# Optimization experiments

Hardware: AMD Instinct MI355X
Metric: run time of the kernel (lower is better)

The kernel has to match this reference:

```python
import jax, jax.numpy as jnp
import numpy as np
from jax import lax

K = 11  # kernel_size
THRESH = 0.2  # focus_threshold default
DN = ('NCHW', 'OIHW', 'NCHW')


def conv3(x, w, b):
    # 3x3 conv, stride 1, SAME padding (padding=1 in torch)
    return lax.conv_general_dilated(x, w, (1, 1), 'SAME', dimension_numbers=DN) + b[None, :, None, None]


def apply_separable_filters(rgb, kh, kv, k):
    # rgb [B,3,H,W]; kh, kv [B,k,H,W] softmaxed per-pixel 1D kernels
    pad = k // 2
    B, C, H, W = rgb.shape
    # horizontal pass: gather k horizontally-shifted views, weight by kh
    xp = jnp.pad(rgb, ((0, 0), (0, 0), (0, 0), (pad, pad)))
    ph = jnp.stack([xp[:, :, :, i:i + W] for i in range(k)], axis=2)  # [B,3,k,H,W]
    h = jnp.einsum('bckhw,bkhw->bchw', ph, kh)
    # vertical pass
    hp = jnp.pad(h, ((0, 0), (0, 0), (pad, pad), (0, 0)))
    pv = jnp.stack([hp[:, :, i:i + H, :] for i in range(k)], axis=2)  # [B,3,k,H,W]
    return jnp.einsum('bckhw,bkhw->bchw', pv, kv)


def get_depth_mask(depth, threshold):
    # binary in-focus mask: pixels closer than threshold stay sharp
    return (depth > threshold).astype(depth.dtype)


def setup_inputs() -> dict:
    key = jax.random.key(0)
    ks = jax.random.split(key, 18)
    B, H, W = 8, 256, 256
    s = 0.05
    f32 = jnp.float32
    inp = {
        'rgb': jax.random.uniform(ks[0], (B, 3, H, W), f32),
        'depth': jax.random.uniform(ks[1], (B, 1, H, W), f32),
        'w1': jax.random.normal(ks[2], (64, 4, 3, 3), f32) * s, 'b1': jnp.zeros(64, f32),
        'w2': jax.random.normal(ks[3], (64, 64, 3, 3), f32) * s, 'b2': jnp.zeros(64, f32),
        'w3': jax.random.normal(ks[4], (128, 64, 3, 3), f32) * s, 'b3': jnp.zeros(128, f32),
        'w4': jax.random.normal(ks[5], (128, 128, 3, 3), f32) * s, 'b4': jnp.zeros(128, f32),
        'w5': jax.random.normal(ks[6], (64, 128, 3, 3), f32) * s, 'b5': jnp.zeros(64, f32),
        'wh': jax.random.normal(ks[7], (K, 64, 3, 3), f32) * s, 'bh': jnp.zeros(K, f32),
        'wv': jax.random.normal(ks[8], (K, 64, 3, 3), f32) * s, 'bv': jnp.zeros(K, f32),
    }
    return inp


def reference(rgb, depth, w1, b1, w2, b2, w3, b3, w4, b4, w5, b5, wh, bh, wv, bv):
    x = jnp.concatenate([rgb, depth], axis=1)  # [B,4,H,W]
    f = jax.nn.relu(conv3(x, w1, b1))
    f = jax.nn.relu(conv3(f, w2, b2))
    f = jax.nn.relu(conv3(f, w3, b3))
    f = jax.nn.relu(conv3(f, w4, b4))
    f = jax.nn.relu(conv3(f, w5, b5))
    kh = jax.nn.softmax(conv3(f, wh, bh), axis=1)
    kv = jax.nn.softmax(conv3(f, wv, bv), axis=1)
    blurred = apply_separable_filters(rgb, kh, kv, K)
    mask = get_depth_mask(depth, THRESH)
    final = mask * rgb + (1.0 - mask) * blurred
    return (final, blurred, kh, kv, mask)
```

## Files before the change

kernel.cpp:

```cpp
#include <hip/hip_runtime.h>
#include <hip/hip_bf16.h>
#include <math.h>

#define HH 256
#define WW 256
#define HW (HH*WW)
#define BB 8

typedef __hip_bfloat16 bf16;
typedef __attribute__((ext_vector_type(8))) short short8;
typedef __attribute__((ext_vector_type(4))) float f32x4;
typedef __attribute__((ext_vector_type(16))) float f32x16;

#define AS1 __attribute__((address_space(1)))
#define AS3 __attribute__((address_space(3)))


template<int CO, int CI>
__global__ __launch_bounds__(256) void reorder_w_cl(const float* __restrict__ w,
                                                    bf16* __restrict__ wr)
{
    int idx = blockIdx.x * 256 + threadIdx.x;
    if (idx >= 9 * CO * CI) return;
    int j    = idx & 7;
    int lane = (idx >> 3) & 63;
    int nt   = (idx >> 9) % (CO / 32);
    int rest = idx / (512 * (CO / 32));
    int ks   = rest & 1;
    int tt   = (rest >> 1) % 9;
    int kc   = rest / 18;
    int co = nt * 32 + (lane & 31);
    int ci = kc * 32 + ks * 16 + (lane >> 5) * 8 + j;
    wr[idx] = __float2bfloat16(w[((size_t)co * CI + ci) * 9 + tt]);
}

__global__ __launch_bounds__(256) void reorder_w_head2_lm(const float* __restrict__ wh,
                                                          const float* __restrict__ wv,
                                                          bf16* __restrict__ wr)
{
    int idx = blockIdx.x * 256 + threadIdx.x;
    if (idx >= 2 * 9 * 2 * 64 * 8) return;
    int j    = idx & 7;
    int lane = (idx >> 3) & 63;
    int fr   = (idx >> 9) & 1;
    int t    = (idx >> 10) % 9;
    int kc   = (idx >> 10) / 9;
    int co   = fr * 16 + (lane & 15);
    int ci   = kc * 32 + (lane >> 4) * 8 + j;
    const float* src = (co < 16) ? wh : wv;
    int c = co & 15;
    float v = (c < 11) ? src[((size_t)c * 64 + ci) * 9 + t] : 0.0f;
    wr[idx] = __float2bfloat16(v);
}

template<int ROWS, int TPB>
__device__ __forceinline__ void zero_oob(bf16* __restrict__ s0,
                                         bf16* __restrict__ s1,
                                         int tid, int x0, int y0)
{
    constexpr int UNITS = (ROWS + 2) * 264;
    const short8 z8 = {0,0,0,0,0,0,0,0};
    for (int e = tid; e < UNITS; e += TPB) {
        int row = e / 264, rem = e - row * 264;
        int px = rem >> 2;
        int yy = y0 - 1 + row, xx = x0 - 1 + px;
        if (yy < 0 || yy >= HH || xx < 0 || xx >= WW) {
            *(short8*)(s0 + (size_t)e * 8) = z8;
            *(short8*)(s1 + (size_t)e * 8) = z8;
        }
    }
}

template<int CIN, int ROWS, int TPB>
__device__ __forceinline__ void stage_async(const bf16* __restrict__ in_i,
                                            bf16* __restrict__ slab,
                                            int tid, int x0, int y0, int k0)
{
    constexpr int UNITS = (ROWS + 2) * 264;
    const int lane = tid & 63;
    const int wb   = tid - lane;
    for (int base = wb; base < UNITS; base += TPB) {
        int e = base + lane;
        int row = e / 264, rem = e - row * 264;
        int px = rem >> 2, slot = rem & 3;
        int seg = slot ^ ((px >> 1) & 3);
        int yy = y0 - 1 + row, xx = x0 - 1 + px;
        bool ok = (e < UNITS) && (yy >= 0) && (yy < HH) && (xx >= 0) && (xx < WW);
        if (ok) {
            const bf16* g = in_i + ((size_t)(yy * WW + xx)) * CIN + k0 + seg * 8;
            __builtin_amdgcn_global_load_lds((const AS1 void*)g,
                                             (AS3 void*)(slab + (size_t)base * 8),
                                             16, 0, 0);
        }
    }
}

template<int COC>
__global__ __launch_bounds__(256) void conv3x3_first(const float* __restrict__ rgb,
                                                     const float* __restrict__ depth,
                                                     const float* __restrict__ w,
                                                     const float* __restrict__ bias,
                                                     bf16* __restrict__ out, int b0)
{
    const int tid = threadIdx.x;
    const int img = blockIdx.y >> 6;
    const int b   = b0 + img;
    const int x = blockIdx.x * 64 + (tid & 63);
    const int y = (blockIdx.y & 63) * 4 + (tid >> 6);

    const bool vy0 = (y > 0), vy2 = (y < HH - 1);
    const bool vx0 = (x > 0), vx2 = (x < WW - 1);
    bool val[9];
    int  off[9];
    {
        int t = 0;
        for (int dy = -1; dy <= 1; ++dy)
            for (int dx = -1; dx <= 1; ++dx) {
                val[t] = (dy < 0 ? vy0 : (dy > 0 ? vy2 : true)) &&
                         (dx < 0 ? vx0 : (dx > 0 ? vx2 : true));
                off[t] = dy * WW + dx;
                ++t;
            }
    }

    float acc[COC];
#pragma unroll
    for (int j = 0; j < COC; ++j) acc[j] = bias[j];

    const int p0 = y * WW + x;
#pragma unroll
    for (int ci = 0; ci < 4; ++ci) {
        const float* p = (ci < 3) ? (rgb + ((size_t)(b * 3 + ci)) * HW + p0)
                                  : (depth + (size_t)b * HW + p0);
        float v[9];
#pragma unroll
        for (int t = 0; t < 9; ++t)
            v[t] = val[t] ? p[off[t]] : 0.0f;

        const float* wp = w + (size_t)ci * 9;
#pragma unroll
        for (int j = 0; j < COC; ++j) {
            const float* wj = wp + (size_t)j * 4 * 9;
#pragma unroll
            for (int t = 0; t < 9; ++t)
                acc[j] = fmaf(wj[t], v[t], acc[j]);
        }
    }

    bf16* op = out + (size_t)img * HW * 64 + (size_t)p0 * 64;
#pragma unroll
    for (int g = 0; g < COC / 8; ++g) {
        short8 s;
#pragma unroll
        for (int j = 0; j < 8; ++j) {
            bf16 h = __float2bfloat16(fmaxf(acc[g * 8 + j], 0.0f));
            s[j] = *reinterpret_cast<short*>(&h);
        }
        *(short8*)(op + g * 8) = s;
    }
}

template<int CIN, int COUT, int WPB>
__global__ __launch_bounds__(256, WPB) void conv_mfma_v12(const bf16* __restrict__ in,
                                                          const bf16* __restrict__ wrb,
                                                          const float* __restrict__ bias,
                                                          bf16* __restrict__ out)
{
    constexpr int NCH  = CIN / 32;
    constexpr int NTT  = COUT / 64;
    constexpr int NTOT = COUT / 32;
    constexpr int SLAB = 6 * 66 * 32;
    __shared__ bf16 slab[2 * SLAB];

    const int tid  = threadIdx.x;
    const int lane = tid & 63;
    const int wv   = tid >> 6;
    const int ng   = wv & 1;
    const int rg   = wv >> 1;
    const int ln31 = lane & 31;
    const int oct  = lane >> 5;
    const int img  = blockIdx.y >> 6;
    const int x0   = blockIdx.x * 64;
    const int y0   = (blockIdx.y & 63) * 4;

    const bf16* in_i  = in  + (size_t)img * HW * CIN;
    bf16*       out_i = out + (size_t)img * HW * COUT;

    f32x16 acc[4][NTT];
#pragma unroll
    for (int mt = 0; mt < 4; ++mt)
#pragma unroll
        for (int nt = 0; nt < NTT; ++nt)
#pragma unroll
            for (int j = 0; j < 16; ++j) acc[mt][nt][j] = 0.0f;

    zero_oob<4, 256>(slab, slab + SLAB, tid, x0, y0);
    stage_async<CIN, 4, 256>(in_i, slab, tid, x0, y0, 0);

    int cur = 0;
    for (int kc = 0; kc < NCH; ++kc) {
        __syncthreads();
        if (kc + 1 < NCH)
            stage_async<CIN, 4, 256>(in_i, slab + (size_t)(cur ^ 1) * SLAB,
                                     tid, x0, y0, (kc + 1) * 32);

        const bf16* sb = slab + (size_t)cur * SLAB;
#pragma unroll
        for (int t = 0; t < 9; ++t) {
            const int dy = t / 3 - 1, dx = t % 3 - 1;
#pragma unroll
            for (int ks = 0; ks < 2; ++ks) {
                short8 a[4];
#pragma unroll
                for (int mt = 0; mt < 4; ++mt) {
                    const int srow = 2 * rg + (mt >> 1) + dy + 1;
                    const int px   = (mt & 1) * 32 + ln31 + dx + 1;
                    const int slot = (ks * 2 + oct) ^ ((px >> 1) & 3);
                    a[mt] = *(const short8*)(sb + (srow * 66 + px) * 32 + slot * 8);
                }
#pragma unroll
                for (int nt = 0; nt < NTT; ++nt) {
                    const int gnt = ng * NTT + nt;
                    short8 bfr = *(const short8*)(wrb
                        + ((size_t)((((kc * 9 + t) * 2 + ks) * NTOT + gnt) * 64 + lane)) * 8);
#pragma unroll
                    for (int mt = 0; mt < 4; ++mt)
                        acc[mt][nt] = __builtin_amdgcn_mfma_f32_32x32x16_bf16(
                                          a[mt], bfr, acc[mt][nt], 0, 0, 0);
                }
            }
        }
        cur ^= 1;
    }

#pragma unroll
    for (int nt = 0; nt < NTT; ++nt) {
        const int co = (ng * NTT + nt) * 32 + ln31;
        const float bb = bias[co];
#pragma unroll
        for (int mt = 0; mt < 4; ++mt) {
            const int r  = 2 * rg + (mt >> 1);
            const int xb = x0 + (mt & 1) * 32;
#pragma unroll
            for (int j = 0; j < 16; ++j) {
                const int m = (j & 3) + 8 * (j >> 2) + 4 * oct;
                const float v = fmaxf(acc[mt][nt][j] + bb, 0.0f);
                out_i[((size_t)(y0 + r) * WW + (xb + m)) * COUT + co] = __float2bfloat16(v);
            }
        }
    }
}

template<int CIN, int COUT, int WPB>
__global__ __launch_bounds__(256, WPB) void conv_mfma_v13(const bf16* __restrict__ in,
                                                          const bf16* __restrict__ wrb,
                                                          const float* __restrict__ bias,
                                                          bf16* __restrict__ out)
{
    constexpr int NCH  = CIN / 32;
    constexpr int NTT  = COUT / 64;
    constexpr int NTOT = COUT / 32;
    constexpr int SLAB = 6 * 66 * 32;
    __shared__ bf16 slab[2 * SLAB];

    const int tid  = threadIdx.x;
    const int lane = tid & 63;
    const int wv   = tid >> 6;
    const int ng   = wv & 1;
    const int rg   = wv >> 1;
    const int ln31 = lane & 31;
    const int oct  = lane >> 5;
    const int img  = blockIdx.y >> 6;
    const int x0   = blockIdx.x * 64;
    const int y0   = (blockIdx.y & 63) * 4;

    const bf16* in_i  = in  + (size_t)img * HW * CIN;
    bf16*       out_i = out + (size_t)img * HW * COUT;

    f32x16 acc[4][NTT];
#pragma unroll
    for (int mt = 0; mt < 4; ++mt)
#pragma unroll
        for (int nt = 0; nt < NTT; ++nt)
#pragma unroll
            for (int j = 0; j < 16; ++j) acc[mt][nt][j] = 0.0f;

    zero_oob<4, 256>(slab, slab + SLAB, tid, x0, y0);
    stage_async<CIN, 4, 256>(in_i, slab, tid, x0, y0, 0);

    int cur = 0;
    for (int kc = 0; kc < NCH; ++kc) {
        __syncthreads();
        if (kc + 1 < NCH)
            stage_async<CIN, 4, 256>(in_i, slab + (size_t)(cur ^ 1) * SLAB,
                                     tid, x0, y0, (kc + 1) * 32);

        const bf16* sb = slab + (size_t)cur * SLAB;
#pragma unroll
        for (int dxi = 0; dxi < 3; ++dxi) {
            const int dx = dxi - 1;
#pragma unroll
            for (int ks = 0; ks < 2; ++ks) {
                short8 af[4][2];
#pragma unroll
                for (int s = 0; s < 4; ++s)
#pragma unroll
                    for (int mx = 0; mx < 2; ++mx) {
                        const int px   = mx * 32 + ln31 + dx + 1;
                        const int slot = (ks * 2 + oct) ^ ((px >> 1) & 3);
                        af[s][mx] = *(const short8*)(sb + ((2 * rg + s) * 66 + px) * 32 + slot * 8);
                    }
#pragma unroll
                for (int dyi = 0; dyi < 3; ++dyi) {
                    const int t = dyi * 3 + dxi;
#pragma unroll
                    for (int nt = 0; nt < NTT; ++nt) {
                        const int gnt = ng * NTT + nt;
                        short8 bfr = *(const short8*)(wrb
                            + ((size_t)((((kc * 9 + t) * 2 + ks) * NTOT + gnt) * 64 + lane)) * 8);
#pragma unroll
                        for (int mt = 0; mt < 4; ++mt)
                            acc[mt][nt] = __builtin_amdgcn_mfma_f32_32x32x16_bf16(
                                              af[(mt >> 1) + dyi][mt & 1], bfr, acc[mt][nt], 0, 0, 0);
                    }
                }
            }
        }
        cur ^= 1;
    }

#pragma unroll
    for (int nt = 0; nt < NTT; ++nt) {
        const int co = (ng * NTT + nt) * 32 + ln31;
        const float bb = bias[co];
#pragma unroll
        for (int mt = 0; mt < 4; ++mt) {
            const int r  = 2 * rg + (mt >> 1);
            const int xb = x0 + (mt & 1) * 32;
#pragma unroll
            for (int j = 0; j < 16; ++j) {
                const int m = (j & 3) + 8 * (j >> 2) + 4 * oct;
                const float v = fmaxf(acc[mt][nt][j] + bb, 0.0f);
                out_i[((size_t)(y0 + r) * WW + (xb + m)) * COUT + co] = __float2bfloat16(v);
            }
        }
    }
}

__global__ __launch_bounds__(256, 2) void head_mfma2(const bf16* __restrict__ in,
                                                     const bf16* __restrict__ wrp,
                                                     const float* __restrict__ bh,
                                                     const float* __restrict__ bv,
                                                     float* __restrict__ kh_base,
                                                     float* __restrict__ kv_base,
                                                     int b0)
{
    constexpr int SLABH = 6 * 66 * 32;
    __shared__ bf16  slab[2 * SLABH];
    __shared__ float smx[4][64][17];

    const int tid  = threadIdx.x;
    const int lane = tid & 63;
    const int wv   = tid >> 6;
    const int m    = lane & 15;
    const int q    = lane >> 4;
    const int img  = blockIdx.y >> 6;
    const int x0   = blockIdx.x * 64;
    const int y0   = (blockIdx.y & 63) * 4;
    const int y    = y0 + wv;

    const bf16* in_i = in + (size_t)img * HW * 64;

    f32x4 acc[4][2];
#pragma unroll
    for (int f = 0; f < 4; ++f) { acc[f][0] = (f32x4){0.f,0.f,0.f,0.f}; acc[f][1] = (f32x4){0.f,0.f,0.f,0.f}; }

    zero_oob<4, 256>(slab, slab + SLABH, tid, x0, y0);
    stage_async<64, 4, 256>(in_i, slab, tid, x0, y0, 0);

    int cur = 0;
    for (int kc = 0; kc < 2; ++kc) {
        __syncthreads();
        if (kc == 0)
            stage_async<64, 4, 256>(in_i, slab + SLABH, tid, x0, y0, 32);

        const bf16* sb = slab + (size_t)cur * SLABH;
#pragma unroll
        for (int t = 0; t < 9; ++t) {
            const int dy = t / 3 - 1, dx = t % 3 - 1;
            const int srow = wv + dy + 1;
            short8 b0f = *(const short8*)(wrp + ((size_t)(((kc * 9 + t) * 2 + 0) * 64 + lane)) * 8);
            short8 b1f = *(const short8*)(wrp + ((size_t)(((kc * 9 + t) * 2 + 1) * 64 + lane)) * 8);
#pragma unroll
            for (int f = 0; f < 4; ++f) {
                const int px = f * 16 + m + dx + 1;
                const int slot = q ^ ((px >> 1) & 3);
                short8 a = *(const short8*)(sb + (srow * 66 + px) * 32 + slot * 8);
                acc[f][0] = __builtin_amdgcn_mfma_f32_16x16x32_bf16(a, b0f, acc[f][0], 0, 0, 0);
                acc[f][1] = __builtin_amdgcn_mfma_f32_16x16x32_bf16(a, b1f, acc[f][1], 0, 0, 0);
            }
        }
        cur ^= 1;
    }

#pragma unroll
    for (int head = 0; head < 2; ++head) {
        const float* bias = head ? bv : bh;
        const float bb = (m < 11) ? bias[m] : 0.0f;
#pragma unroll
        for (int f = 0; f < 4; ++f)
#pragma unroll
            for (int r = 0; r < 4; ++r)
                smx[wv][f * 16 + q * 4 + r][m] = acc[f][head][r] + bb;

        float v[11];
#pragma unroll
        for (int j = 0; j < 11; ++j) v[j] = smx[wv][lane][j];
        float mx = v[0];
#pragma unroll
        for (int j = 1; j < 11; ++j) mx = fmaxf(mx, v[j]);
        float s = 0.0f;
#pragma unroll
        for (int j = 0; j < 11; ++j) { v[j] = expf(v[j] - mx); s += v[j]; }
        const float inv = 1.0f / s;

        float* op = (head ? kv_base : kh_base) + (size_t)(b0 + img) * 11 * HW
                    + (size_t)y * WW + x0 + lane;
#pragma unroll
        for (int j = 0; j < 11; ++j)
            op[(size_t)j * HW] = v[j] * inv;
    }
}

__global__ __launch_bounds__(256) void hpass(const float* __restrict__ rgb,
                                             const float* __restrict__ kh,
                                             float* __restrict__ h)
{
    int idx = blockIdx.x * 256 + threadIdx.x;
    int b = idx >> 16;
    int p = idx & (HW - 1);
    int y = p >> 8;
    int x = p & 255;

    float kw[11];
#pragma unroll
    for (int i = 0; i < 11; ++i) kw[i] = kh[((size_t)(b * 11 + i)) * HW + p];

#pragma unroll
    for (int c = 0; c < 3; ++c) {
        const float* rp = rgb + ((size_t)(b * 3 + c)) * HW + (size_t)y * WW;
        float s = 0.0f;
#pragma unroll
        for (int i = 0; i < 11; ++i) {
            int xx = x + i - 5;
            if (xx >= 0 && xx < WW) s = fmaf(kw[i], rp[xx], s);
        }
        h[((size_t)(b * 3 + c)) * HW + p] = s;
    }
}

__global__ __launch_bounds__(256) void vpass_compose(const float* __restrict__ h,
                                                     const float* __restrict__ kv,
                                                     const float* __restrict__ rgb,
                                                     const float* __restrict__ depth,
                                                     float* __restrict__ fin,
                                                     float* __restrict__ blur,
                                                     float* __restrict__ masko)
{
    int idx = blockIdx.x * 256 + threadIdx.x;
    int b = idx >> 16;
    int p = idx & (HW - 1);
    int y = p >> 8;
    int x = p & 255;

    float kw[11];
#pragma unroll
    for (int i = 0; i < 11; ++i) kw[i] = kv[((size_t)(b * 11 + i)) * HW + p];

    float d = depth[idx];
    float mk = (d > 0.2f) ? 1.0f : 0.0f;
    masko[idx] = mk;

#pragma unroll
    for (int c = 0; c < 3; ++c) {
        const float* hp = h + ((size_t)(b * 3 + c)) * HW + x;
        float s = 0.0f;
#pragma unroll
        for (int i = 0; i < 11; ++i) {
            int yy = y + i - 5;
            if (yy >= 0 && yy < HH) s = fmaf(kw[i], hp[(size_t)yy * WW], s);
        }
        size_t o = ((size_t)(b * 3 + c)) * HW + p;
        blur[o] = s;
        fin[o] = mk * rgb[o] + (1.0f - mk) * s;
    }
}

extern "C" void kernel_launch(void* const* d_in, const int* in_sizes, int n_in,
                              void* d_out, int out_size, void* d_ws, size_t ws_size,
                              hipStream_t stream)
{
    const float* rgb   = (const float*)d_in[0];
    const float* depth = (const float*)d_in[1];
    const float* w1 = (const float*)d_in[2];  const float* b1 = (const float*)d_in[3];
    const float* w2 = (const float*)d_in[4];  const float* b2 = (const float*)d_in[5];
    const float* w3 = (const float*)d_in[6];  const float* b3 = (const float*)d_in[7];
    const float* w4 = (const float*)d_in[8];  const float* b4 = (const float*)d_in[9];
    const float* w5 = (const float*)d_in[10]; const float* b5 = (const float*)d_in[11];
    const float* wh = (const float*)d_in[12]; const float* bh = (const float*)d_in[13];
    const float* wv = (const float*)d_in[14]; const float* bv = (const float*)d_in[15];

    float* out    = (float*)d_out;
    float* fin_o  = out;
    float* blur_o = out + 1572864;
    float* kh_o   = out + 3145728;
    float* kv_o   = out + 8912896;
    float* mask_o = out + 14680064;

    const size_t perG = (size_t)HW * 2 * (128 + 64 + 128);
    const size_t wsz  = (size_t)1 * 1024 * 1024;
    int G = 1;
    if (ws_size >= 8 * perG + wsz) G = 8;
    else if (ws_size >= 4 * perG + wsz) G = 4;
    else if (ws_size >= 2 * perG + wsz) G = 2;

    char* ws = (char*)d_ws;
    const size_t szA = (size_t)G * HW * 128 * 2;
    const size_t szB = (size_t)G * HW * 64 * 2;
    const size_t szC = (size_t)G * HW * 128 * 2;
    bf16* bufA = (bf16*)ws;
    bf16* bufB = (bf16*)(ws + szA);
    bf16* bufC = (bf16*)(ws + szA + szB);
    float* hbuf = (float*)bufC;

    bf16* w2r  = (bf16*)(ws + szA + szB + szC);
    bf16* w3r  = w2r + 9 * 64 * 64;
    bf16* w4r  = w3r + 9 * 128 * 64;
    bf16* w5r  = w4r + 9 * 128 * 128;
    bf16* whvr = w5r + 9 * 64 * 128;

    dim3 blk(256);

    reorder_w_cl<64, 64>  <<<dim3((9*64*64   + 255) / 256), blk, 0, stream>>>(w2, w2r);
    reorder_w_cl<128, 64> <<<dim3((9*128*64  + 255) / 256), blk, 0, stream>>>(w3, w3r);
    reorder_w_cl<128, 128><<<dim3((9*128*128 + 255) / 256), blk, 0, stream>>>(w4, w4r);
    reorder_w_cl<64, 128> <<<dim3((9*64*128  + 255) / 256), blk, 0, stream>>>(w5, w5r);
    reorder_w_head2_lm    <<<dim3((18432     + 255) / 256), blk, 0, stream>>>(wh, wv, whvr);

    for (int b0 = 0; b0 < BB; b0 += G) {
        conv3x3_first<64><<<dim3(4, 64 * G, 1), blk, 0, stream>>>(rgb, depth, w1, b1, bufA, b0);
        conv_mfma_v13<64, 64, 3>  <<<dim3(4, 64 * G), blk, 0, stream>>>(bufA, w2r, b2, bufB);
        conv_mfma_v12<64, 128, 2> <<<dim3(4, 64 * G), blk, 0, stream>>>(bufB, w3r, b3, bufC);
        conv_mfma_v12<128, 128, 2><<<dim3(4, 64 * G), blk, 0, stream>>>(bufC, w4r, b4, bufA);
        conv_mfma_v13<128, 64, 3> <<<dim3(4, 64 * G), blk, 0, stream>>>(bufA, w5r, b5, bufB);
        head_mfma2<<<dim3(4, 64 * G), blk, 0, stream>>>(bufB, whvr, bh, bv, kh_o, kv_o, b0);
    }

    hpass<<<dim3(2048), blk, 0, stream>>>(rgb, kh_o, hbuf);
    vpass_compose<<<dim3(2048), blk, 0, stream>>>(hbuf, kv_o, rgb, depth,
                                                  fin_o, blur_o, mask_o);
}
```

Measured before the change: 777.5 us.

## Move first conv to MFMA via padded 8-channel bf16 input and reordered weights

Replaces the scalar FMA first 3x3 conv (4 input channels to 64) with a pre-pass that writes a zero-padded 258x258 bf16 image holding 8 channels per pixel (RGB, depth, zeros). An MFMA kernel then packs two taps per 16-wide K step and runs 5 K steps of 32x32x16 bf16 MFMA. This removes the per-thread 36x64 FMA loop and the boundary checks. In exchange it adds an extra kernel launch and a padded buffer write and read, reuses the bufC workspace as the padded buffer, and writes output with scattered 2-byte stores.

```diff
diff --git a/kernel.cpp b/kernel.cpp
--- a/kernel.cpp
+++ b/kernel.cpp
@@ -6,6 +6,8 @@
 #define WW 256
 #define HW (HH*WW)
 #define BB 8
+#define PW 258
+#define PHW2 (PW*PW)
 
 typedef __hip_bfloat16 bf16;
 typedef __attribute__((ext_vector_type(8))) short short8;
@@ -51,6 +53,113 @@
     int c = co & 15;
     float v = (c < 11) ? src[((size_t)c * 64 + ci) * 9 + t] : 0.0f;
     wr[idx] = __float2bfloat16(v);
+}
+
+__global__ __launch_bounds__(256) void reorder_w1_mfma(const float* __restrict__ w,
+                                                       bf16* __restrict__ wr)
+{
+    int idx = blockIdx.x * 256 + threadIdx.x;
+    if (idx >= 5 * 2 * 64 * 8) return;
+    int j    = idx & 7;
+    int lane = (idx >> 3) & 63;
+    int nt   = (idx >> 9) & 1;
+    int km   = idx >> 10;
+    int co   = nt * 32 + (lane & 31);
+    int tap  = km * 2 + (lane >> 5);
+    float v  = (tap < 9 && j < 4) ? w[((size_t)co * 4 + j) * 9 + tap] : 0.0f;
+    wr[idx] = __float2bfloat16(v);
+}
+
+__global__ __launch_bounds__(256) void pad8_rgbd(const float* __restrict__ rgb,
+                                                 const float* __restrict__ depth,
+                                                 bf16* __restrict__ p8,
+                                                 int b0, int G)
+{
+    int idx = blockIdx.x * 256 + threadIdx.x;
+    if (idx >= G * PHW2) return;
+    int img = idx / PHW2;
+    int rem = idx - img * PHW2;
+    int r = rem / PW, c = rem - r * PW;
+    int y = r - 1, x = c - 1;
+    short8 s = {0,0,0,0,0,0,0,0};
+    if (y >= 0 && y < HH && x >= 0 && x < WW) {
+        const int b = b0 + img;
+        const int p0 = y * WW + x;
+        float v[4];
+        v[0] = rgb[((size_t)(b * 3 + 0)) * HW + p0];
+        v[1] = rgb[((size_t)(b * 3 + 1)) * HW + p0];
+        v[2] = rgb[((size_t)(b * 3 + 2)) * HW + p0];
+        v[3] = depth[(size_t)b * HW + p0];
+#pragma unroll
+        for (int j = 0; j < 4; ++j) {
+            bf16 h = __float2bfloat16(v[j]);
+            s[j] = *reinterpret_cast<short*>(&h);
+        }
+    }
+    *(short8*)(p8 + (size_t)idx * 8) = s;
+}
+
+__global__ __launch_bounds__(256, 3) void conv1_mfma(const bf16* __restrict__ p8,
+                                                     const bf16* __restrict__ w1r,
+                                                     const float* __restrict__ bias,
+                                                     bf16* __restrict__ out)
+{
+    const int tid  = threadIdx.x;
+    const int lane = tid & 63;
+    const int wv   = tid >> 6;
+    const int ln31 = lane & 31;
+    const int oct  = lane >> 5;
+    const int img  = blockIdx.y >> 6;
+    const int x0   = blockIdx.x * 64;
+    const int y    = (blockIdx.y & 63) * 4 + wv;
+
+    const bf16* p8i   = p8  + (size_t)img * PHW2 * 8;
+    bf16*       out_i = out + (size_t)img * HW * 64;
+
+    f32x16 acc[2][2];
+#pragma unroll
+    for (int mt = 0; mt < 2; ++mt)
+#pragma unroll
+        for (int nt = 0; nt < 2; ++nt)
+#pragma unroll
+            for (int j = 0; j < 16; ++j) acc[mt][nt][j] = 0.0f;
+
+#pragma unroll
+    for (int km = 0; km < 5; ++km) {
+        const int tap = km * 2 + oct;
+        const int te  = (tap < 9) ? tap : 8;
+        const int dy  = te / 3 - 1, dx = te % 3 - 1;
+        short8 a[2];
+#pragma unroll
+        for (int mt = 0; mt < 2; ++mt) {
+            const int px = x0 + mt * 32 + ln31 + dx + 1;
+            a[mt] = *(const short8*)(p8i + ((size_t)(y + dy + 1) * PW + px) * 8);
+        }
+#pragma unroll
+        for (int nt = 0; nt < 2; ++nt) {
+            short8 bfr = *(const short8*)(w1r + ((size_t)((km * 2 + nt) * 64 + lane)) * 8);
+#pragma unroll
+            for (int mt = 0; mt < 2; ++mt)
+                acc[mt][nt] = __builtin_amdgcn_mfma_f32_32x32x16_bf16(
+                                  a[mt], bfr, acc[mt][nt], 0, 0, 0);
+        }
+    }
+
+#pragma unroll
+    for (int nt = 0; nt < 2; ++nt) {
+        const int co = nt * 32 + ln31;
+        const float bb = bias[co];
+#pragma unroll
+        for (int mt = 0; mt < 2; ++mt) {
+            const int xb = x0 + mt * 32;
+#pragma unroll
+            for (int j = 0; j < 16; ++j) {
+                const int m = (j & 3) + 8 * (j >> 2) + 4 * oct;
+                const float v = fmaxf(acc[mt][nt][j] + bb, 0.0f);
+                out_i[((size_t)y * WW + (xb + m)) * 64 + co] = __float2bfloat16(v);
+            }
+        }
+    }
 }
 
 template<int ROWS, int TPB>
@@ -95,71 +204,6 @@
     }
 }
 
-template<int COC>
-__global__ __launch_bounds__(256) void conv3x3_first(const float* __restrict__ rgb,
-                                                     const float* __restrict__ depth,
-                                                     const float* __restrict__ w,
-                                                     const float* __restrict__ bias,
-                                                     bf16* __restrict__ out, int b0)
-{
-    const int tid = threadIdx.x;
-    const int img = blockIdx.y >> 6;
-    const int b   = b0 + img;
-    const int x = blockIdx.x * 64 + (tid & 63);
-    const int y = (blockIdx.y & 63) * 4 + (tid >> 6);
-
-    const bool vy0 = (y > 0), vy2 = (y < HH - 1);
-    const bool vx0 = (x > 0), vx2 = (x < WW - 1);
-    bool val[9];
-    int  off[9];
-    {
-        int t = 0;
-        for (int dy = -1; dy <= 1; ++dy)
-            for (int dx = -1; dx <= 1; ++dx) {
-                val[t] = (dy < 0 ? vy0 : (dy > 0 ? vy2 : true)) &&
-                         (dx < 0 ? vx0 : (dx > 0 ? vx2 : true));
-                off[t] = dy * WW + dx;
-                ++t;
-            }
-    }
-
-    float acc[COC];
-#pragma unroll
-    for (int j = 0; j < COC; ++j) acc[j] = bias[j];
-
-    const int p0 = y * WW + x;
-#pragma unroll
-    for (int ci = 0; ci < 4; ++ci) {
-        const float* p = (ci < 3) ? (rgb + ((size_t)(b * 3 + ci)) * HW + p0)
-                                  : (depth + (size_t)b * HW + p0);
-        float v[9];
-#pragma unroll
-        for (int t = 0; t < 9; ++t)
-            v[t] = val[t] ? p[off[t]] : 0.0f;
-
-        const float* wp = w + (size_t)ci * 9;
-#pragma unroll
-        for (int j = 0; j < COC; ++j) {
-            const float* wj = wp + (size_t)j * 4 * 9;
-#pragma unroll
-            for (int t = 0; t < 9; ++t)
-                acc[j] = fmaf(wj[t], v[t], acc[j]);
-        }
-    }
-
-    bf16* op = out + (size_t)img * HW * 64 + (size_t)p0 * 64;
-#pragma unroll
-    for (int g = 0; g < COC / 8; ++g) {
-        short8 s;
-#pragma unroll
-        for (int j = 0; j < 8; ++j) {
-            bf16 h = __float2bfloat16(fmaxf(acc[g * 8 + j], 0.0f));
-            s[j] = *reinterpret_cast<short*>(&h);
-        }
-        *(short8*)(op + g * 8) = s;
-    }
-}
-
 template<int CIN, int COUT, int WPB>
 __global__ __launch_bounds__(256, WPB) void conv_mfma_v12(const bf16* __restrict__ in,
                                                           const bf16* __restrict__ wrb,
@@ -532,12 +576,14 @@
     bf16* bufB = (bf16*)(ws + szA);
     bf16* bufC = (bf16*)(ws + szA + szB);
     float* hbuf = (float*)bufC;
+    bf16*  p8   = (bf16*)bufC;
 
     bf16* w2r  = (bf16*)(ws + szA + szB + szC);
     bf16* w3r  = w2r + 9 * 64 * 64;
     bf16* w4r  = w3r + 9 * 128 * 64;
     bf16* w5r  = w4r + 9 * 128 * 128;
     bf16* whvr = w5r + 9 * 64 * 128;
+    bf16* w1r  = whvr + 18432;
 
     dim3 blk(256);
 
@@ -546,9 +592,11 @@
     reorder_w_cl<128, 128><<<dim3((9*128*128 + 255) / 256), blk, 0, stream>>>(w4, w4r);
     reorder_w_cl<64, 128> <<<dim3((9*64*128  + 255) / 256), blk, 0, stream>>>(w5, w5r);
     reorder_w_head2_lm    <<<dim3((18432     + 255) / 256), blk, 0, stream>>>(wh, wv, whvr);
+    reorder_w1_mfma       <<<dim3((5120      + 255) / 256), blk, 0, stream>>>(w1, w1r);
 
     for (int b0 = 0; b0 < BB; b0 += G) {
-        conv3x3_first<64><<<dim3(4, 64 * G, 1), blk, 0, stream>>>(rgb, depth, w1, b1, bufA, b0);
+        pad8_rgbd <<<dim3((G * PHW2 + 255) / 256), blk, 0, stream>>>(rgb, depth, p8, b0, G);
+        conv1_mfma<<<dim3(4, 64 * G), blk, 0, stream>>>(p8, w1r, b1, bufA);
         conv_mfma_v13<64, 64, 3>  <<<dim3(4, 64 * G), blk, 0, stream>>>(bufA, w2r, b2, bufB);
         conv_mfma_v12<64, 128, 2> <<<dim3(4, 64 * G), blk, 0, stream>>>(bufB, w3r, b3, bufC);
         conv_mfma_v12<128, 128, 2><<<dim3(4, 64 * G), blk, 0, stream>>>(bufC, w4r, b4, bufA);
```

New measurement: 647.1 us. 16.8% less time.
